# Performance work log

Measured on AMD Instinct MI355X. Metric: run time of the kernel, lower is better.

Reference implementation:

```python
import jax, jax.numpy as jnp
import numpy as np


def _warp2d_transpose(grad_out, u):
    """Adjoint of bilinear warp with zero boundary handling.

    grad_out: [B,H,W,C] incoming gradient (channel-last)
    u:        [B,H,W,2] flow, u[...,0]=dx (horizontal), u[...,1]=dy (vertical)
    Returns grad_x: [B,H,W,C] via flow-guided bilinear scatter-add.
    """
    B, H, W, C = grad_out.shape
    yy, xx = jnp.meshgrid(jnp.arange(H, dtype=grad_out.dtype),
                          jnp.arange(W, dtype=grad_out.dtype), indexing='ij')
    gx = xx[None] + u[..., 0]  # [B,H,W] sample x-coord
    gy = yy[None] + u[..., 1]  # [B,H,W] sample y-coord
    x0f = jnp.floor(gx)
    y0f = jnp.floor(gy)
    wx = gx - x0f  # fractional weights
    wy = gy - y0f
    x0 = x0f.astype(jnp.int32)
    y0 = y0f.astype(jnp.int32)
    x1 = x0 + 1
    y1 = y0 + 1
    bidx = jnp.arange(B, dtype=jnp.int32)[:, None, None]  # broadcast batch index

    grad_x = jnp.zeros((B, H, W, C), dtype=grad_out.dtype)
    corners = (
        (y0, x0, (1.0 - wy) * (1.0 - wx)),
        (y0, x1, (1.0 - wy) * wx),
        (y1, x0, wy * (1.0 - wx)),
        (y1, x1, wy * wx),
    )
    for yi, xi, w in corners:
        valid = (xi >= 0) & (xi < W) & (yi >= 0) & (yi < H)  # mode='zeros'
        w = jnp.where(valid, w, 0.0)
        xi = jnp.clip(xi, 0, W - 1)
        yi = jnp.clip(yi, 0, H - 1)
        grad_x = grad_x.at[bidx, yi, xi].add(w[..., None] * grad_out)
    return grad_x


def setup_inputs() -> dict:
    key = jax.random.key(0)
    k1, k2, k3 = jax.random.split(key, 3)
    B, H, W, C = 8, 512, 512, 16
    grad_out = jax.random.normal(k1, (B, H, W, C), dtype=jnp.float32)
    u = jax.random.normal(k2, (B, H, W, 2), dtype=jnp.float32) * 4.0
    x = jax.random.normal(k3, (B, H, W, C), dtype=jnp.float32)
    return {"grad_out": grad_out, "u": u, "x": x}


def reference(grad_out, u, x):
    # channel_last=True: the TF layer transposes to NCHW, calls the kernel,
    # and transposes back; in jax we keep NHWC throughout (same math).
    # x only determines the output shape/dtype of the adjoint.
    return _warp2d_transpose(grad_out, u)
```

## Files before the change

kernel.cpp:

```cpp
#include <hip/hip_runtime.h>

#define BB 8
#define HH 512
#define WW 512
#define CC 16

__global__ __launch_bounds__(256) void zero_fill_f4(float4* __restrict__ p, int n4)
{
    int i = blockIdx.x * 256 + threadIdx.x;
    if (i < n4) p[i] = make_float4(0.f, 0.f, 0.f, 0.f);
}

__global__ __launch_bounds__(256) void warp_transpose_scatter(
    const float* __restrict__ gout,
    const float* __restrict__ u,
    float* __restrict__ gx)
{
    const int gid = blockIdx.x * 256 + threadIdx.x;
    const int c   = gid & (CC - 1);
    const int p   = gid >> 4;
    const int x   = p & (WW - 1);
    const int y   = (p >> 9) & (HH - 1);
    const int b   = p >> 18;

    const float2 uv = reinterpret_cast<const float2*>(u)[p];
    const float sx = (float)x + uv.x;
    const float sy = (float)y + uv.y;
    const float x0f = floorf(sx);
    const float y0f = floorf(sy);
    const float wx = sx - x0f;
    const float wy = sy - y0f;
    const int x0 = (int)x0f;
    const int y0 = (int)y0f;
    const int x1 = x0 + 1;
    const int y1 = y0 + 1;

    const float g   = gout[gid];
    const float w00 = (1.0f - wy) * (1.0f - wx) * g;
    const float w01 = (1.0f - wy) * wx * g;
    const float w10 = wy * (1.0f - wx) * g;
    const float w11 = wy * wx * g;

    const bool vx0 = (unsigned)x0 < (unsigned)WW;
    const bool vx1 = (unsigned)x1 < (unsigned)WW;
    const bool vy0 = (unsigned)y0 < (unsigned)HH;
    const bool vy1 = (unsigned)y1 < (unsigned)HH;

    const int base = b * (HH * WW);
    if (vy0 && vx0) atomicAdd(&gx[((base + y0 * WW + x0) << 4) + c], w00);
    if (vy0 && vx1) atomicAdd(&gx[((base + y0 * WW + x1) << 4) + c], w01);
    if (vy1 && vx0) atomicAdd(&gx[((base + y1 * WW + x0) << 4) + c], w10);
    if (vy1 && vx1) atomicAdd(&gx[((base + y1 * WW + x1) << 4) + c], w11);
}

extern "C" void kernel_launch(void* const* d_in, const int* in_sizes, int n_in,
                              void* d_out, int out_size, void* d_ws, size_t ws_size,
                              hipStream_t stream) {
    const float* gout = (const float*)d_in[0];
    const float* u    = (const float*)d_in[1];
    float* gx = (float*)d_out;

    const int total = BB * HH * WW * CC;
    const int n4    = total / 4;
    zero_fill_f4<<<(n4 + 255) / 256, 256, 0, stream>>>((float4*)gx, n4);

    const int blocks = total / 256;
    warp_transpose_scatter<<<blocks, 256, 0, stream>>>(gout, u, gx);
}
```

Baseline: 638.2 us.

## Replace float atomic scatter with binned integer-atomic index pass and gather

The float-atomic scatter of all 16 channels per corner is replaced by two passes. First, each source pixel claims a slot at each of its valid target pixels with one integer atomic and stores a packed offset/corner code there; the output buffer itself serves as the bin storage. A gather pass then recomputes the bilinear weights and accumulates the float4 channels per target pixel without atomics. Entries that exceed the 15 slots or the ±127 offset range go to a workspace overflow list, applied afterwards with float atomics. This cuts atomic traffic sharply and adds a control-flow-heavy gather with scattered reads of flow and gradient; if the workspace is absent, overflow entries are silently dropped. Block indices are also remapped across the 8 XCDs.

```diff
diff --git a/kernel.cpp b/kernel.cpp
--- a/kernel.cpp
+++ b/kernel.cpp
@@ -4,6 +4,10 @@
 #define HH 512
 #define WW 512
 #define CC 16
+#define NPIX (BB * HH * WW)
+#define NTOT (NPIX * CC)
+#define KSLOTS 15
+#define NXCD 8
 
 __global__ __launch_bounds__(256) void zero_fill_f4(float4* __restrict__ p, int n4)
 {
@@ -11,59 +15,157 @@
     if (i < n4) p[i] = make_float4(0.f, 0.f, 0.f, 0.f);
 }
 
-__global__ __launch_bounds__(256) void warp_transpose_scatter(
+__global__ void zero_ws(unsigned* __restrict__ ws)
+{
+    if (threadIdx.x == 0) ws[0] = 0u;
+}
+
+__device__ __forceinline__ void push_ovf(unsigned* ws, int cap,
+                                         unsigned q, unsigned p, float w)
+{
+    if (cap <= 0) return;
+    unsigned idx = atomicAdd(&ws[0], 1u);
+    if ((int)idx < cap) {
+        unsigned* e = ws + 4 + 3u * idx;
+        e[0] = q;
+        e[1] = p;
+        e[2] = __float_as_uint(w);
+    }
+}
+
+__global__ __launch_bounds__(256) void bin_pass(
+    const float2* __restrict__ u2,
+    unsigned* __restrict__ bins,
+    unsigned* __restrict__ ws, int ovf_cap)
+{
+    int bid = blockIdx.x;
+    bid = (bid & (NXCD - 1)) * (NPIX / 256 / NXCD) + (bid >> 3);
+
+    const int p     = bid * 256 + threadIdx.x;
+    const int x     = p & (WW - 1);
+    const int y     = (p >> 9) & (HH - 1);
+    const int pbase = p & ~(HH * WW - 1);
+
+    const float2 uv  = u2[p];
+    const float  sx  = (float)x + uv.x;
+    const float  sy  = (float)y + uv.y;
+    const float  x0f = floorf(sx);
+    const float  y0f = floorf(sy);
+    const int    x0  = (int)x0f;
+    const int    y0  = (int)y0f;
+    const float  wx  = sx - x0f;
+    const float  wy  = sy - y0f;
+
+#pragma unroll
+    for (int cy = 0; cy < 2; ++cy) {
+        const int Y = y0 + cy;
+        if ((unsigned)Y >= (unsigned)HH) continue;
+#pragma unroll
+        for (int cx = 0; cx < 2; ++cx) {
+            const int X = x0 + cx;
+            if ((unsigned)X >= (unsigned)WW) continue;
+            const int q  = pbase + Y * WW + X;
+            const int dx = x - X;
+            const int dy = y - Y;
+            if (dx < -127 || dx > 127 || dy < -127 || dy > 127) {
+                const float w = (cx ? wx : 1.f - wx) * (cy ? wy : 1.f - wy);
+                push_ovf(ws, ovf_cap, (unsigned)q, (unsigned)p, w);
+                continue;
+            }
+            const unsigned slot = atomicAdd(&bins[(unsigned)q << 4], 1u);
+            if (slot < KSLOTS) {
+                bins[((unsigned)q << 4) + 1 + slot] =
+                    (unsigned)(cx | (cy << 1) | ((dx + 128) << 2) | ((dy + 128) << 10));
+            } else {
+                const float w = (cx ? wx : 1.f - wx) * (cy ? wy : 1.f - wy);
+                push_ovf(ws, ovf_cap, (unsigned)q, (unsigned)p, w);
+            }
+        }
+    }
+}
+
+__global__ __launch_bounds__(256) void gather_pass(
+    const float4* __restrict__ gout4,
+    const float2* __restrict__ u2,
+    float* gx)
+{
+    int bid = blockIdx.x;
+    bid = (bid & (NXCD - 1)) * (NPIX * 4 / 256 / NXCD) + (bid >> 3);
+
+    const int t     = bid * 256 + threadIdx.x;
+    const int c4    = t & 3;
+    const int q     = t >> 2;
+    const int X     = q & (WW - 1);
+    const int Y     = (q >> 9) & (HH - 1);
+    const int pbase = q & ~(HH * WW - 1);
+
+    const unsigned* bins = (const unsigned*)gx;
+
+    unsigned cnt = bins[(unsigned)q << 4];
+    if (cnt > KSLOTS) cnt = KSLOTS;
+
+    float4 acc = make_float4(0.f, 0.f, 0.f, 0.f);
+    for (unsigned j = 0; j < cnt; ++j) {
+        const unsigned e  = bins[((unsigned)q << 4) + 1 + j];
+        const int cx = e & 1;
+        const int cy = (e >> 1) & 1;
+        const int dx = (int)((e >> 2) & 255) - 128;
+        const int dy = (int)((e >> 10) & 255) - 128;
+        const int xp = X + dx;
+        const int yp = Y + dy;
+        const int p  = pbase + yp * WW + xp;
+
+        const float2 uv  = u2[p];
+        const float  sxp = (float)xp + uv.x;
+        const float  syp = (float)yp + uv.y;
+        const float  wx  = sxp - floorf(sxp);
+        const float  wy  = syp - floorf(syp);
+        const float  w   = (cx ? wx : 1.f - wx) * (cy ? wy : 1.f - wy);
+
+        const float4 g = gout4[(p << 2) + c4];
+        acc.x += w * g.x;
+        acc.y += w * g.y;
+        acc.z += w * g.z;
+        acc.w += w * g.w;
+    }
+    reinterpret_cast<float4*>(gx)[t] = acc;
+}
+
+__global__ __launch_bounds__(256) void ovf_pass(
     const float* __restrict__ gout,
-    const float* __restrict__ u,
-    float* __restrict__ gx)
+    const unsigned* __restrict__ ws,
+    float* __restrict__ gx, int cap)
 {
-    const int gid = blockIdx.x * 256 + threadIdx.x;
-    const int c   = gid & (CC - 1);
-    const int p   = gid >> 4;
-    const int x   = p & (WW - 1);
-    const int y   = (p >> 9) & (HH - 1);
-    const int b   = p >> 18;
-
-    const float2 uv = reinterpret_cast<const float2*>(u)[p];
-    const float sx = (float)x + uv.x;
-    const float sy = (float)y + uv.y;
-    const float x0f = floorf(sx);
-    const float y0f = floorf(sy);
-    const float wx = sx - x0f;
-    const float wy = sy - y0f;
-    const int x0 = (int)x0f;
-    const int y0 = (int)y0f;
-    const int x1 = x0 + 1;
-    const int y1 = y0 + 1;
-
-    const float g   = gout[gid];
-    const float w00 = (1.0f - wy) * (1.0f - wx) * g;
-    const float w01 = (1.0f - wy) * wx * g;
-    const float w10 = wy * (1.0f - wx) * g;
-    const float w11 = wy * wx * g;
-
-    const bool vx0 = (unsigned)x0 < (unsigned)WW;
-    const bool vx1 = (unsigned)x1 < (unsigned)WW;
-    const bool vy0 = (unsigned)y0 < (unsigned)HH;
-    const bool vy1 = (unsigned)y1 < (unsigned)HH;
-
-    const int base = b * (HH * WW);
-    if (vy0 && vx0) atomicAdd(&gx[((base + y0 * WW + x0) << 4) + c], w00);
-    if (vy0 && vx1) atomicAdd(&gx[((base + y0 * WW + x1) << 4) + c], w01);
-    if (vy1 && vx0) atomicAdd(&gx[((base + y1 * WW + x0) << 4) + c], w10);
-    if (vy1 && vx1) atomicAdd(&gx[((base + y1 * WW + x1) << 4) + c], w11);
+    unsigned n = ws[0];
+    if (n > (unsigned)cap) n = (unsigned)cap;
+    const unsigned total  = n * 16u;
+    const unsigned stride = gridDim.x * blockDim.x;
+    for (unsigned i = blockIdx.x * blockDim.x + threadIdx.x; i < total; i += stride) {
+        const unsigned e = i >> 4;
+        const unsigned c = i & 15u;
+        const unsigned q = ws[4 + 3u * e];
+        const unsigned p = ws[4 + 3u * e + 1];
+        const float    w = __uint_as_float(ws[4 + 3u * e + 2]);
+        atomicAdd(&gx[(q << 4) + c], w * gout[(p << 4) + c]);
+    }
 }
 
 extern "C" void kernel_launch(void* const* d_in, const int* in_sizes, int n_in,
                               void* d_out, int out_size, void* d_ws, size_t ws_size,
-                              hipStream_t stream) {
+                              hipStream_t stream)
+{
     const float* gout = (const float*)d_in[0];
     const float* u    = (const float*)d_in[1];
-    float* gx = (float*)d_out;
+    float*    gx = (float*)d_out;
+    unsigned* ws = (unsigned*)d_ws;
 
-    const int total = BB * HH * WW * CC;
-    const int n4    = total / 4;
-    zero_fill_f4<<<(n4 + 255) / 256, 256, 0, stream>>>((float4*)gx, n4);
+    const int cap = (ws && ws_size >= 64) ? (int)((ws_size - 16) / 12) : 0;
 
-    const int blocks = total / 256;
-    warp_transpose_scatter<<<blocks, 256, 0, stream>>>(gout, u, gx);
+    zero_fill_f4<<<NTOT / 4 / 256, 256, 0, stream>>>((float4*)gx, NTOT / 4);
+    if (cap > 0) zero_ws<<<1, 64, 0, stream>>>(ws);
+
+    bin_pass<<<NPIX / 256, 256, 0, stream>>>((const float2*)u, (unsigned*)gx, ws, cap);
+    gather_pass<<<NPIX * 4 / 256, 256, 0, stream>>>((const float4*)gout,
+                                                    (const float2*)u, gx);
+    if (cap > 0) ovf_pass<<<256, 256, 0, stream>>>(gout, ws, gx, cap);
 }
```

Result: slower. 1.085 ms (+70.0%).

## Replace global atomic scatter with per-row shared-memory gather plus outlier pass

Applied to the files above, without the earlier changes.

Each block owns one output row of one image. It scans a window of nearby source rows, queues pixels whose vertical sample falls on that row, and accumulates their contributions with shared-memory atomics before a plain vectorized store. This removes the separate zero-fill and most global atomics. A second kernel handles the rare pixels whose vertical displacement exceeds the window using global atomics. The cost is redundant reads of the flow field across overlapping windows and a reliance on flow magnitudes being mostly within the window.

```diff
diff --git a/kernel.cpp b/kernel.cpp
--- a/kernel.cpp
+++ b/kernel.cpp
@@ -4,66 +4,151 @@
 #define HH 512
 #define WW 512
 #define CC 16
+#define HW (HH * WW)
+#define RWIN 16
+#define QCAP 1024
 
-__global__ __launch_bounds__(256) void zero_fill_f4(float4* __restrict__ p, int n4)
+__global__ __launch_bounds__(256) void row_gather(
+    const float* __restrict__ gout,
+    const float2* __restrict__ u2,
+    float4* __restrict__ gx4)
 {
-    int i = blockIdx.x * 256 + threadIdx.x;
-    if (i < n4) p[i] = make_float4(0.f, 0.f, 0.f, 0.f);
+    const int img = blockIdx.x & 7;
+    const int Y   = blockIdx.x >> 3;
+    const int tid = threadIdx.x;
+
+    __shared__ float    acc[WW * CC];
+    __shared__ unsigned q[QCAP];
+    __shared__ unsigned qn;
+
+    float4* acc4 = (float4*)acc;
+#pragma unroll
+    for (int i = 0; i < (WW * CC / 4) / 256; ++i)
+        acc4[tid + i * 256] = make_float4(0.f, 0.f, 0.f, 0.f);
+    if (tid == 0) qn = 0u;
+    __syncthreads();
+
+    const float Yf  = (float)Y;
+    const float Ym1 = Yf - 1.0f;
+    const int   ylo = (Y - RWIN < 0) ? 0 : Y - RWIN;
+    const int   yhi = (Y + RWIN > HH - 1) ? HH - 1 : Y + RWIN;
+    const int   ibase = img * HW;
+
+    for (int yp0 = ylo; yp0 <= yhi; yp0 += 2) {
+#pragma unroll
+        for (int dy = 0; dy < 2; ++dy) {
+            const int yp = yp0 + dy;
+            if (yp > yhi) continue;
+#pragma unroll
+            for (int half = 0; half < 2; ++half) {
+                const int x = half * 256 + tid;
+                const float2 uv = u2[ibase + yp * WW + x];
+                const float sy  = (float)yp + uv.y;
+                const float y0f = floorf(sy);
+                if (y0f == Yf || y0f == Ym1) {
+                    const unsigned pos = atomicAdd(&qn, 1u);
+                    q[pos] = (unsigned)((yp << 16) | x);
+                }
+            }
+        }
+        __syncthreads();
+
+        const unsigned n   = qn;
+        const int      grp = tid >> 4;
+        const int      c   = tid & 15;
+        for (unsigned e = (unsigned)grp; e < n; e += 16u) {
+            const unsigned ent = q[e];
+            const int ys = (int)(ent >> 16);
+            const int xs = (int)(ent & 0xffffu);
+            const int p  = ibase + ys * WW + xs;
+            const float2 uv = u2[p];
+            const float sy   = (float)ys + uv.y;
+            const float y0f  = floorf(sy);
+            const float fy   = sy - y0f;
+            const float wrow = (y0f == Yf) ? (1.0f - fy) : fy;
+            const float sx   = (float)xs + uv.x;
+            const float x0f  = floorf(sx);
+            const float wx   = sx - x0f;
+            const float g    = gout[p * CC + c] * wrow;
+            if (x0f >= 0.0f && x0f <= (float)(WW - 1)) {
+                const int x0 = (int)x0f;
+                atomicAdd(&acc[(x0 << 4) + c], g * (1.0f - wx));
+            }
+            if (x0f >= -1.0f && x0f <= (float)(WW - 2)) {
+                const int x1 = (int)x0f + 1;
+                atomicAdd(&acc[(x1 << 4) + c], g * wx);
+            }
+        }
+        __syncthreads();
+        if (tid == 0) qn = 0u;
+        __syncthreads();
+    }
+
+    const int obase = (ibase + Y * WW) * CC / 4;
+#pragma unroll
+    for (int i = 0; i < (WW * CC / 4) / 256; ++i)
+        gx4[obase + tid + i * 256] = acc4[tid + i * 256];
 }
 
-__global__ __launch_bounds__(256) void warp_transpose_scatter(
+__global__ __launch_bounds__(256) void outlier_pass(
     const float* __restrict__ gout,
-    const float* __restrict__ u,
+    const float2* __restrict__ u2,
     float* __restrict__ gx)
 {
-    const int gid = blockIdx.x * 256 + threadIdx.x;
-    const int c   = gid & (CC - 1);
-    const int p   = gid >> 4;
-    const int x   = p & (WW - 1);
-    const int y   = (p >> 9) & (HH - 1);
-    const int b   = p >> 18;
+    const int p = blockIdx.x * 256 + threadIdx.x;
+    const int x = p & (WW - 1);
+    const int y = (p >> 9) & (HH - 1);
 
-    const float2 uv = reinterpret_cast<const float2*>(u)[p];
-    const float sx = (float)x + uv.x;
-    const float sy = (float)y + uv.y;
+    const float2 uv  = u2[p];
+    const float  sy  = (float)y + uv.y;
+    const float  y0f = floorf(sy);
+    const float  fy  = sy - y0f;
+    const float  yF  = (float)y;
+    const float  R   = (float)RWIN;
+
+    const bool m0 = (y0f >= 0.0f)  && (y0f <= (float)(HH - 1)) && fabsf(y0f - yF) > R;
+    const bool m1 = (y0f >= -1.0f) && (y0f <= (float)(HH - 2)) && fabsf(y0f + 1.0f - yF) > R;
+    if (!m0 && !m1) return;
+
+    const float sx  = (float)x + uv.x;
     const float x0f = floorf(sx);
-    const float y0f = floorf(sy);
-    const float wx = sx - x0f;
-    const float wy = sy - y0f;
-    const int x0 = (int)x0f;
-    const int y0 = (int)y0f;
-    const int x1 = x0 + 1;
-    const int y1 = y0 + 1;
+    const float wx  = sx - x0f;
+    const bool vx0 = (x0f >= 0.0f)  && (x0f <= (float)(WW - 1));
+    const bool vx1 = (x0f >= -1.0f) && (x0f <= (float)(WW - 2));
+    if (!vx0 && !vx1) return;
 
-    const float g   = gout[gid];
-    const float w00 = (1.0f - wy) * (1.0f - wx) * g;
-    const float w01 = (1.0f - wy) * wx * g;
-    const float w10 = wy * (1.0f - wx) * g;
-    const float w11 = wy * wx * g;
-
-    const bool vx0 = (unsigned)x0 < (unsigned)WW;
-    const bool vx1 = (unsigned)x1 < (unsigned)WW;
-    const bool vy0 = (unsigned)y0 < (unsigned)HH;
-    const bool vy1 = (unsigned)y1 < (unsigned)HH;
-
-    const int base = b * (HH * WW);
-    if (vy0 && vx0) atomicAdd(&gx[((base + y0 * WW + x0) << 4) + c], w00);
-    if (vy0 && vx1) atomicAdd(&gx[((base + y0 * WW + x1) << 4) + c], w01);
-    if (vy1 && vx0) atomicAdd(&gx[((base + y1 * WW + x0) << 4) + c], w10);
-    if (vy1 && vx1) atomicAdd(&gx[((base + y1 * WW + x1) << 4) + c], w11);
+    const int ibase = p & ~(HW - 1);
+    const int gbase = p * CC;
+#pragma unroll
+    for (int k = 0; k < 2; ++k) {
+        const bool mm = k ? m1 : m0;
+        if (!mm) continue;
+        const float wr = k ? fy : (1.0f - fy);
+        const int   r  = (int)y0f + k;
+        const int rowb = (ibase + r * WW) * CC;
+        if (vx0) {
+            const int   x0 = (int)x0f;
+            const float w  = wr * (1.0f - wx);
+            for (int c = 0; c < CC; ++c)
+                atomicAdd(&gx[rowb + (x0 << 4) + c], w * gout[gbase + c]);
+        }
+        if (vx1) {
+            const int   x1 = (int)x0f + 1;
+            const float w  = wr * wx;
+            for (int c = 0; c < CC; ++c)
+                atomicAdd(&gx[rowb + (x1 << 4) + c], w * gout[gbase + c]);
+        }
+    }
 }
 
 extern "C" void kernel_launch(void* const* d_in, const int* in_sizes, int n_in,
                               void* d_out, int out_size, void* d_ws, size_t ws_size,
-                              hipStream_t stream) {
+                              hipStream_t stream)
+{
     const float* gout = (const float*)d_in[0];
     const float* u    = (const float*)d_in[1];
     float* gx = (float*)d_out;
 
-    const int total = BB * HH * WW * CC;
-    const int n4    = total / 4;
-    zero_fill_f4<<<(n4 + 255) / 256, 256, 0, stream>>>((float4*)gx, n4);
-
-    const int blocks = total / 256;
-    warp_transpose_scatter<<<blocks, 256, 0, stream>>>(gout, u, gx);
+    row_gather<<<BB * HH, 256, 0, stream>>>(gout, (const float2*)u, (float4*)gx);
+    outlier_pass<<<(BB * HW) / 256, 256, 0, stream>>>(gout, (const float2*)u, gx);
 }
```

New measurement: 948.8 us. 1.49x slower.
